# Kernel optimization log

Measured on AMD Instinct MI355X. Metric: run time of the kernel, lower is better.

## Reference

```python
import jax, jax.numpy as jnp
import numpy as np

DIM = 3072
HEADS = 24
HEAD_DIM = 128
SEQ = 4096
BATCH = 1
EPS = 1e-6


def setup_inputs() -> dict:
    key = jax.random.key(0)
    ks = jax.random.split(key, 12)
    s = 1.0 / np.sqrt(DIM)
    return {
        "hidden_states": jax.random.normal(ks[0], (BATCH, SEQ, DIM), dtype=jnp.float32),
        "cos": jax.random.uniform(ks[1], (SEQ, HEAD_DIM), dtype=jnp.float32, minval=-1.0, maxval=1.0),
        "sin": jax.random.uniform(ks[2], (SEQ, HEAD_DIM), dtype=jnp.float32, minval=-1.0, maxval=1.0),
        "Wq": jax.random.normal(ks[3], (DIM, HEADS * HEAD_DIM), dtype=jnp.float32) * s,
        "bq": jax.random.normal(ks[4], (HEADS * HEAD_DIM,), dtype=jnp.float32) * 0.02,
        "Wk": jax.random.normal(ks[5], (DIM, HEADS * HEAD_DIM), dtype=jnp.float32) * s,
        "bk": jax.random.normal(ks[6], (HEADS * HEAD_DIM,), dtype=jnp.float32) * 0.02,
        "Wv": jax.random.normal(ks[7], (DIM, HEADS * HEAD_DIM), dtype=jnp.float32) * s,
        "bv": jax.random.normal(ks[8], (HEADS * HEAD_DIM,), dtype=jnp.float32) * 0.02,
        "gq": jnp.ones((HEAD_DIM,), dtype=jnp.float32),
        "gk": jnp.ones((HEAD_DIM,), dtype=jnp.float32),
    }


def _rms_norm(x, g):
    # RMSNorm over last dim (head_dim), learnable scale g
    var = jnp.mean(jnp.square(x), axis=-1, keepdims=True)
    return x * jax.lax.rsqrt(var + EPS) * g


def _apply_rope(x, cos, sin):
    # x: [B, S, H, D]; cos/sin: [S, D]. Interleaved-pair rotation (Flux style).
    xr = x.reshape(*x.shape[:-1], HEAD_DIM // 2, 2)
    x_rot = jnp.stack((-xr[..., 1], xr[..., 0]), axis=-1).reshape(x.shape)
    c = cos[None, :, None, :]
    s = sin[None, :, None, :]
    return x * c + x_rot * s


def reference(hidden_states, cos, sin, Wq, bq, Wk, bk, Wv, bv, gq, gk):
    B, S, _ = hidden_states.shape
    q = (hidden_states @ Wq + bq).reshape(B, S, HEADS, HEAD_DIM)
    k = (hidden_states @ Wk + bk).reshape(B, S, HEADS, HEAD_DIM)
    v = (hidden_states @ Wv + bv).reshape(B, S, HEADS, HEAD_DIM)
    q = _apply_rope(_rms_norm(q, gq), cos, sin)
    k = _apply_rope(_rms_norm(k, gk), cos, sin)
    scale = 1.0 / jnp.sqrt(jnp.asarray(HEAD_DIM, dtype=q.dtype))
    scores = jnp.einsum("bqhd,bkhd->bhqk", q, k) * scale  # [B, H, S, S]
    probs = jax.nn.softmax(scores, axis=-1)
    out = jnp.einsum("bhqk,bkhd->bqhd", probs, v)  # [B, S, H, D]
    return out.reshape(B, S, HEADS * HEAD_DIM)
```

## Files before the change

### kernel.cpp

```cpp
#include <hip/hip_runtime.h>
#include <hip/hip_bf16.h>
#include <stdint.h>

#define DIM 3072
#define SEQ 4096
#define NH 24
#define HD 128

typedef __hip_bfloat16 bf16;
typedef __bf16 bfv8 __attribute__((ext_vector_type(8)));
typedef float f32x4 __attribute__((ext_vector_type(4)));
typedef float f32x16 __attribute__((ext_vector_type(16)));
typedef unsigned short us4 __attribute__((ext_vector_type(4)));
typedef unsigned short us8 __attribute__((ext_vector_type(8)));

template <int N> struct ic { static constexpr int value = N; };

__device__ __forceinline__ void async16(void* lds, const void* g) {
  __builtin_amdgcn_global_load_lds((const __attribute__((address_space(1))) void*)g,
                                   (__attribute__((address_space(3))) void*)lds, 16, 0, 0);
}

__device__ __forceinline__ unsigned short f2bf(float f) {
  unsigned int u = __builtin_bit_cast(unsigned int, f);
  u += 0x7fffu + ((u >> 16) & 1u);
  return (unsigned short)(u >> 16);
}
__device__ __forceinline__ float bf2f(unsigned short b) {
  return __builtin_bit_cast(float, (unsigned int)b << 16);
}
__device__ __forceinline__ unsigned int cvtpk(float lo, float hi) {
  unsigned int r;
  asm("v_cvt_pk_bf16_f32 %0, %1, %2" : "=v"(r) : "v"(lo), "v"(hi));
  return r;
}
__device__ __forceinline__ void pl32swap(unsigned int& a, unsigned int& b) {
  asm volatile("v_permlane32_swap_b32 %0, %1" : "+v"(a), "+v"(b));
}
#if __has_builtin(__builtin_amdgcn_exp2f)
__device__ __forceinline__ float fexp2(float x) { return __builtin_amdgcn_exp2f(x); }
#else
__device__ __forceinline__ float fexp2(float x) { return exp2f(x); }
#endif

#define MFMA16(a, b, c) __builtin_amdgcn_mfma_f32_16x16x32_bf16((a), (b), (c), 0, 0, 0)
#define MFMA32(a, b, c) __builtin_amdgcn_mfma_f32_32x32x16_bf16((a), (b), (c), 0, 0, 0)

__global__ __launch_bounds__(256) void k_cast(const float4* __restrict__ in,
                                              us4* __restrict__ o, int n4) {
  int i = blockIdx.x * 256 + threadIdx.x;
  if (i >= n4) return;
  float4 v = in[i];
  us4 r;
  r.x = f2bf(v.x); r.y = f2bf(v.y); r.z = f2bf(v.z); r.w = f2bf(v.w);
  o[i] = r;
}

__global__ __launch_bounds__(256) void k_transW(const float* __restrict__ W0,
    const float* __restrict__ W1, const float* __restrict__ W2,
    unsigned short* __restrict__ T0, unsigned short* __restrict__ T1,
    unsigned short* __restrict__ T2) {
  int z = blockIdx.z;
  const float* W = (z == 0) ? W0 : (z == 1) ? W1 : W2;
  unsigned short* T = (z == 0) ? T0 : (z == 1) ? T1 : T2;
  int kb = blockIdx.y * 64;
  int nb = blockIdx.x * 64;
  __shared__ float tile[64 * 64];
  int t = threadIdx.x;
#pragma unroll
  for (int p = 0; p < 4; ++p) {
    int cid = p * 256 + t;
    int row = cid >> 4, c4 = cid & 15;
    int slot = (c4 + (row >> 3)) & 15;
    float4 v = *(const float4*)&W[(size_t)(kb + row) * DIM + nb + c4 * 4];
    *(float4*)&tile[row * 64 + slot * 4] = v;
  }
  __syncthreads();
#pragma unroll
  for (int p = 0; p < 2; ++p) {
    int cid = p * 256 + t;
    int nl = cid >> 3, c8 = cid & 7;
    us8 o;
#pragma unroll
    for (int j = 0; j < 8; ++j) {
      int k = c8 * 8 + j;
      int slot = ((nl >> 2) + (k >> 3)) & 15;
      o[j] = f2bf(tile[k * 64 + slot * 4 + (nl & 3)]);
    }
    *(us8*)&T[(size_t)(nb + nl) * DIM + kb + c8 * 8] = o;
  }
}

__global__ __launch_bounds__(256, 2) void k_gemm(const unsigned short* __restrict__ A,
    const unsigned short* __restrict__ B0, const unsigned short* __restrict__ B1,
    const unsigned short* __restrict__ B2, const float* __restrict__ c0,
    const float* __restrict__ c1, const float* __restrict__ c2,
    unsigned short* __restrict__ o0, unsigned short* __restrict__ o1,
    unsigned short* __restrict__ o2) {
  const int z = blockIdx.z;
  const unsigned short* Bt = (z == 0) ? B0 : (z == 1) ? B1 : B2;
  const float* bias = (z == 0) ? c0 : (z == 1) ? c1 : c2;
  unsigned short* outp = (z == 0) ? o0 : (z == 1) ? o1 : o2;
  const int nb = blockIdx.x * 128;
  const int mb = blockIdx.y * 128;
  const int t = threadIdx.x;
  const int w = t >> 6, l = t & 63;
  const int wr = w >> 1, wc = w & 1;
  const int lq = l & 15, lg = l >> 4;
  __shared__ unsigned short lA[128 * 64];
  __shared__ unsigned short lB[128 * 64];
  f32x4 acc[4][4];
#pragma unroll
  for (int i = 0; i < 4; ++i)
#pragma unroll
    for (int j = 0; j < 4; ++j) acc[i][j] = (f32x4){0.f, 0.f, 0.f, 0.f};

  for (int kb = 0; kb < DIM; kb += 64) {
    __syncthreads();
#pragma unroll
    for (int r = 0; r < 4; ++r) {
      int row = (w * 4 + r) * 8 + (l >> 3);
      int sl = (l & 7) ^ (row & 7);
      async16(&lA[(w * 4 + r) * 512], A + (size_t)(mb + row) * DIM + kb + sl * 8);
      async16(&lB[(w * 4 + r) * 512], Bt + (size_t)(nb + row) * DIM + kb + sl * 8);
    }
    __syncthreads();
#pragma unroll
    for (int kc = 0; kc < 2; ++kc) {
      bfv8 af[4], bfv[4];
#pragma unroll
      for (int mf = 0; mf < 4; ++mf) {
        int row = wr * 64 + mf * 16 + lq;
        af[mf] = *(const bfv8*)&lA[row * 64 + (((kc * 4 + lg) ^ (row & 7)) * 8)];
      }
#pragma unroll
      for (int nf = 0; nf < 4; ++nf) {
        int row = wc * 64 + nf * 16 + lq;
        bfv[nf] = *(const bfv8*)&lB[row * 64 + (((kc * 4 + lg) ^ (row & 7)) * 8)];
      }
#pragma unroll
      for (int mf = 0; mf < 4; ++mf)
#pragma unroll
        for (int nf = 0; nf < 4; ++nf)
          acc[mf][nf] = MFMA16(af[mf], bfv[nf], acc[mf][nf]);
    }
  }
#pragma unroll
  for (int nf = 0; nf < 4; ++nf) {
    int n = nb + wc * 64 + nf * 16 + lq;
    float bv_ = bias[n];
    int hh = n >> 7, dd = n & 127;
    unsigned short* obase = outp + (size_t)hh * SEQ * HD + dd;
#pragma unroll
    for (int mf = 0; mf < 4; ++mf) {
      int srow = mb + wr * 64 + mf * 16 + lg * 4;
#pragma unroll
      for (int r = 0; r < 4; ++r)
        obase[(size_t)(srow + r) * HD] = f2bf(acc[mf][nf][r] + bv_);
    }
  }
}

__global__ __launch_bounds__(256) void k_rmsrope(unsigned short* __restrict__ qb,
    unsigned short* __restrict__ kbuf, const float* __restrict__ cosT,
    const float* __restrict__ sinT, const float* __restrict__ gq,
    const float* __restrict__ gk) {
  int rowid = blockIdx.x * 4 + (threadIdx.x >> 6);
  int l = threadIdx.x & 63;
  int which = (rowid >= NH * SEQ) ? 1 : 0;
  int r2 = which ? rowid - NH * SEQ : rowid;
  int hh = r2 >> 12;
  int s = r2 & 4095;
  unsigned short* base = (which ? kbuf : qb) + ((size_t)hh * SEQ + s) * HD + 2 * l;
  const float* g = which ? gk : gq;
  unsigned int u = *(const unsigned int*)base;
  float x0 = bf2f((unsigned short)(u & 0xffffu));
  float x1 = bf2f((unsigned short)(u >> 16));
  float ss = x0 * x0 + x1 * x1;
#pragma unroll
  for (int o = 1; o < 64; o <<= 1) ss += __shfl_xor(ss, o);
  float rr = rsqrtf(ss * (1.0f / 128.0f) + 1e-6f);
  int d0 = 2 * l;
  float c0v = cosT[s * HD + d0], c1v = cosT[s * HD + d0 + 1];
  float s0v = sinT[s * HD + d0], s1v = sinT[s * HD + d0 + 1];
  float y0 = x0 * rr * g[d0];
  float y1 = x1 * rr * g[d0 + 1];
  float o0 = y0 * c0v - y1 * s0v;
  float o1 = y1 * c1v + y0 * s1v;
  if (!which) { o0 *= 0.1275174373f; o1 *= 0.1275174373f; }
  *(unsigned int*)base = (unsigned int)f2bf(o0) | ((unsigned int)f2bf(o1) << 16);
}

__global__ __launch_bounds__(256) void k_transV(const unsigned short* __restrict__ vb,
                                                unsigned short* __restrict__ vt) {
  int hh = blockIdx.y;
  int sb = blockIdx.x * 64;
  __shared__ unsigned short tile[64 * 128];
  int t = threadIdx.x;
#pragma unroll
  for (int p = 0; p < 4; ++p) {
    int cid = p * 256 + t;
    int row = cid >> 4, c = cid & 15;
    int slot = (c + (row >> 3)) & 15;
    us8 v = *(const us8*)&vb[((size_t)hh * SEQ + sb + row) * HD + c * 8];
    *(us8*)&tile[row * 128 + slot * 8] = v;
  }
  __syncthreads();
#pragma unroll
  for (int p = 0; p < 4; ++p) {
    int cid = p * 256 + t;
    int d = cid >> 3, c8 = cid & 7;
    us8 o;
#pragma unroll
    for (int j = 0; j < 8; ++j) {
      int s = c8 * 8 + j;
      int slot = ((d >> 3) + (s >> 3)) & 15;
      o[j] = tile[s * 128 + slot * 8 + (d & 7)];
    }
    *(us8*)&vt[((size_t)hh * HD + d) * SEQ + sb + c8 * 8] = o;
  }
}

__global__ __launch_bounds__(256, 3) void k_attn(const unsigned short* __restrict__ qg,
    const unsigned short* __restrict__ kg, const unsigned short* __restrict__ vtg,
    float* __restrict__ outp) {
  const int h = blockIdx.y;
  const int qb0 = blockIdx.x * 128;
  const int t = threadIdx.x;
  const int w = t >> 6, l = t & 63;
  const int l31 = l & 31, hi = l >> 5;

  __shared__ unsigned short lKf[3 * 4096];
  __shared__ unsigned short lVf[3 * 4096];

  bfv8 qf[8];
  {
    const unsigned short* qrow = qg + ((size_t)h * SEQ + qb0 + w * 32 + l31) * HD + hi * 8;
#pragma unroll
    for (int ks = 0; ks < 8; ++ks) qf[ks] = *(const bfv8*)(qrow + ks * 16);
  }

  int kidx[8], vidx[4][2];
#pragma unroll
  for (int ks = 0; ks < 8; ++ks)
    kidx[ks] = l31 * 128 + (((ks * 2 + hi) ^ (l31 & 7) ^ ((l31 >> 3) & 1)) * 8);
#pragma unroll
  for (int dt = 0; dt < 4; ++dt)
#pragma unroll
    for (int ksub = 0; ksub < 2; ++ksub)
      vidx[dt][ksub] =
          (dt * 32 + l31) * 32 + (((ksub * 2 + hi) ^ (l31 & 3) ^ ((l31 >> 2) & 3)) * 8);

  const unsigned short *kp0, *kp1, *vp0, *vp1;
  {
    int kr0 = w * 4 + (l >> 4), kr1 = 16 + kr0;
    kp0 = kg + ((size_t)h * SEQ + kr0) * HD + (((l & 15) ^ (kr0 & 7) ^ ((kr0 >> 3) & 1)) * 8);
    kp1 = kg + ((size_t)h * SEQ + kr1) * HD + (((l & 15) ^ (kr1 & 7) ^ ((kr1 >> 3) & 1)) * 8);
    int vr0 = w * 16 + (l >> 2), vr1 = 64 + vr0;
    vp0 = vtg + ((size_t)h * HD + vr0) * SEQ + (((l & 3) ^ (vr0 & 3) ^ ((vr0 >> 2) & 3)) * 8);
    vp1 = vtg + ((size_t)h * HD + vr1) * SEQ + (((l & 3) ^ (vr1 & 3) ^ ((vr1 >> 2) & 3)) * 8);
  }

#define STAGE(B)                                                        \
  do {                                                                  \
    async16(&lKf[(B) * 4096 + w * 512], kp0);        kp0 += 32 * HD;    \
    async16(&lKf[(B) * 4096 + 2048 + w * 512], kp1); kp1 += 32 * HD;    \
    async16(&lVf[(B) * 4096 + w * 512], vp0);        vp0 += 32;         \
    async16(&lVf[(B) * 4096 + 2048 + w * 512], vp1); vp1 += 32;         \
  } while (0)

  f32x16 oacc[4];
#pragma unroll
  for (int dt = 0; dt < 4; ++dt)
#pragma unroll
    for (int r = 0; r < 16; ++r) oacc[dt][r] = 0.f;
  float l_run = 0.f;

  STAGE(0);
  STAGE(1);

  auto tile = [&](auto bufc, auto waitc, auto stagec) {
    constexpr int CUR = decltype(bufc)::value;
    constexpr int WAITN = decltype(waitc)::value;
    constexpr int DOSTAGE = decltype(stagec)::value;
    if constexpr (WAITN == 4)
      asm volatile("s_waitcnt vmcnt(4)" ::: "memory");
    else
      asm volatile("s_waitcnt vmcnt(0)" ::: "memory");
    __builtin_amdgcn_s_barrier();
    __builtin_amdgcn_sched_barrier(0);
    if constexpr (DOSTAGE) STAGE((CUR + 2) % 3);
    __builtin_amdgcn_sched_barrier(0);

    f32x16 st;
#pragma unroll
    for (int r = 0; r < 16; ++r) st[r] = 0.f;
    __builtin_amdgcn_s_setprio(1);
#pragma unroll
    for (int ks = 0; ks < 8; ++ks) {
      bfv8 kf = *(const bfv8*)&lKf[CUR * 4096 + kidx[ks]];
      st = MFMA32(kf, qf[ks], st);
    }
    __builtin_amdgcn_s_setprio(0);

#pragma unroll
    for (int r = 0; r < 16; ++r) st[r] = fexp2(st[r]);
    float s01 = st[0] + st[1], s23 = st[2] + st[3];
    float s45 = st[4] + st[5], s67 = st[6] + st[7];
    float s89 = st[8] + st[9], sab = st[10] + st[11];
    float scd = st[12] + st[13], sef = st[14] + st[15];
    float lsum = ((s01 + s23) + (s45 + s67)) + ((s89 + sab) + (scd + sef));
    lsum += __shfl_xor(lsum, 32);
    l_run += lsum;

    bfv8 pa[2];
    {
      unsigned int a0 = cvtpk(st[0], st[1]), a1 = cvtpk(st[2], st[3]);
      unsigned int b0 = cvtpk(st[4], st[5]), b1 = cvtpk(st[6], st[7]);
      unsigned int c0 = cvtpk(st[8], st[9]), c1 = cvtpk(st[10], st[11]);
      unsigned int d0 = cvtpk(st[12], st[13]), d1 = cvtpk(st[14], st[15]);
      pl32swap(a0, b0); pl32swap(a1, b1); pl32swap(c0, d0); pl32swap(c1, d1);
      pa[0] = __builtin_bit_cast(bfv8, make_uint4(a0, a1, b0, b1));
      pa[1] = __builtin_bit_cast(bfv8, make_uint4(c0, c1, d0, d1));
    }

    __builtin_amdgcn_s_setprio(1);
#pragma unroll
    for (int dt = 0; dt < 4; ++dt)
#pragma unroll
      for (int ksub = 0; ksub < 2; ++ksub) {
        bfv8 vf = *(const bfv8*)&lVf[CUR * 4096 + vidx[dt][ksub]];
        oacc[dt] = MFMA32(pa[ksub], vf, oacc[dt]);
      }
    __builtin_amdgcn_s_setprio(0);
  };

  for (int it = 0; it < 42; ++it) {
    tile(ic<0>{}, ic<4>{}, ic<1>{});
    tile(ic<1>{}, ic<4>{}, ic<1>{});
    tile(ic<2>{}, ic<4>{}, ic<1>{});
  }
  tile(ic<0>{}, ic<4>{}, ic<0>{});
  tile(ic<1>{}, ic<0>{}, ic<0>{});

  float linv = 1.0f / l_run;
#pragma unroll
  for (int r = 0; r < 16; ++r) {
    int qr = (r & 3) + 8 * (r >> 2) + 4 * hi;
    float lr = __shfl(linv, qr);
    float* orow = outp + (size_t)(qb0 + w * 32 + qr) * DIM + h * HD;
#pragma unroll
    for (int dt = 0; dt < 4; ++dt) orow[dt * 32 + l31] = oacc[dt][r] * lr;
  }
#undef STAGE
}

extern "C" void kernel_launch(void* const* d_in, const int* in_sizes, int n_in,
                              void* d_out, int out_size, void* d_ws, size_t ws_size,
                              hipStream_t stream) {
  const float* hs = (const float*)d_in[0];
  const float* cosT = (const float*)d_in[1];
  const float* sinT = (const float*)d_in[2];
  const float* Wq = (const float*)d_in[3];
  const float* bq = (const float*)d_in[4];
  const float* Wk = (const float*)d_in[5];
  const float* bk = (const float*)d_in[6];
  const float* Wv = (const float*)d_in[7];
  const float* bv = (const float*)d_in[8];
  const float* gq = (const float*)d_in[9];
  const float* gk = (const float*)d_in[10];
  float* out = (float*)d_out;

  char* ws = (char*)d_ws;
  const size_t SZ_HS = (size_t)SEQ * DIM * 2;
  const size_t SZ_W = (size_t)DIM * DIM * 2;
  const size_t SZ_HEAD = (size_t)NH * SEQ * HD * 2;
  unsigned short* hsb = (unsigned short*)ws;               ws += SZ_HS;
  unsigned short* WqT = (unsigned short*)ws;               ws += SZ_W;
  unsigned short* WkT = (unsigned short*)ws;               ws += SZ_W;
  unsigned short* WvT = (unsigned short*)ws;               ws += SZ_W;
  unsigned short* q_b = (unsigned short*)ws;               ws += SZ_HEAD;
  unsigned short* k_b = (unsigned short*)ws;               ws += SZ_HEAD;
  unsigned short* v_b = (unsigned short*)ws;               ws += SZ_HEAD;
  unsigned short* vtr = (unsigned short*)ws;               ws += SZ_HEAD;

  int n4 = SEQ * DIM / 4;
  k_cast<<<dim3(n4 / 256), dim3(256), 0, stream>>>((const float4*)hs, (us4*)hsb, n4);
  k_transW<<<dim3(48, 48, 3), dim3(256), 0, stream>>>(Wq, Wk, Wv, WqT, WkT, WvT);
  k_gemm<<<dim3(24, 32, 3), dim3(256), 0, stream>>>(hsb, WqT, WkT, WvT, bq, bk, bv,
                                                    q_b, k_b, v_b);
  k_rmsrope<<<dim3(2 * NH * SEQ / 4), dim3(256), 0, stream>>>(q_b, k_b, cosT, sinT, gq, gk);
  k_transV<<<dim3(64, 24), dim3(256), 0, stream>>>(v_b, vtr);
  k_attn<<<dim3(32, 24), dim3(256), 0, stream>>>(q_b, k_b, vtr, out);
}
```

Before: 572.7 us.

## Retile QKV GEMM to 256x256 with triple-buffered async LDS pipeline

The QKV projection GEMM moves from 128x128 tiles with 256 threads and a sync-load-sync loop to 256x256 tiles with 512 threads. It uses a K-step of 32, a three-stage async global-to-LDS ring with vmcnt waits, and a new XOR swizzle. This targets the exposed load latency and barrier stalls, and raises per-block data reuse. Separately, the attention QK^T MFMA chain is split into two independent accumulators to shorten the dependency chain. The larger tile means 576 blocks and more accumulators per thread, which risks register pressure and lower occupancy.

```diff
diff --git a/kernel.cpp b/kernel.cpp
--- a/kernel.cpp
+++ b/kernel.cpp
@@ -91,7 +91,7 @@
   }
 }
 
-__global__ __launch_bounds__(256, 2) void k_gemm(const unsigned short* __restrict__ A,
+__global__ __launch_bounds__(512, 2) void k_gemm(const unsigned short* __restrict__ A,
     const unsigned short* __restrict__ B0, const unsigned short* __restrict__ B1,
     const unsigned short* __restrict__ B2, const float* __restrict__ c0,
     const float* __restrict__ c1, const float* __restrict__ c2,
@@ -101,64 +101,107 @@
   const unsigned short* Bt = (z == 0) ? B0 : (z == 1) ? B1 : B2;
   const float* bias = (z == 0) ? c0 : (z == 1) ? c1 : c2;
   unsigned short* outp = (z == 0) ? o0 : (z == 1) ? o1 : o2;
-  const int nb = blockIdx.x * 128;
-  const int mb = blockIdx.y * 128;
-  const int t = threadIdx.x;
-  const int w = t >> 6, l = t & 63;
-  const int wr = w >> 1, wc = w & 1;
+  const int nb = blockIdx.x * 256;
+  const int mb = blockIdx.y * 256;
+  const int tid = threadIdx.x;
+  const int w = tid >> 6, l = tid & 63;
+  const int wm = w >> 2, wn = w & 3;
   const int lq = l & 15, lg = l >> 4;
-  __shared__ unsigned short lA[128 * 64];
-  __shared__ unsigned short lB[128 * 64];
-  f32x4 acc[4][4];
-#pragma unroll
-  for (int i = 0; i < 4; ++i)
+
+  __shared__ unsigned short lA[3 * 8192];
+  __shared__ unsigned short lB[3 * 8192];
+
+  const int srow0 = tid >> 2, srow1 = 128 + (tid >> 2);
+  const int sc = tid & 3;
+  const unsigned short* ap0 = A + (size_t)(mb + srow0) * DIM + ((sc ^ ((srow0 >> 1) & 3)) * 8);
+  const unsigned short* ap1 = A + (size_t)(mb + srow1) * DIM + ((sc ^ ((srow1 >> 1) & 3)) * 8);
+  const unsigned short* bp0 = Bt + (size_t)(nb + srow0) * DIM + ((sc ^ ((srow0 >> 1) & 3)) * 8);
+  const unsigned short* bp1 = Bt + (size_t)(nb + srow1) * DIM + ((sc ^ ((srow1 >> 1) & 3)) * 8);
+  const int dA0 = w * 512, dA1 = 4096 + w * 512;
+
+#define GSTAGE(B)                                              \
+  do {                                                         \
+    async16(&lA[(B) * 8192 + dA0], ap0); ap0 += 32;            \
+    async16(&lA[(B) * 8192 + dA1], ap1); ap1 += 32;            \
+    async16(&lB[(B) * 8192 + dA0], bp0); bp0 += 32;            \
+    async16(&lB[(B) * 8192 + dA1], bp1); bp1 += 32;            \
+  } while (0)
+
+  int aOff[8], bOff[4];
+#pragma unroll
+  for (int mf = 0; mf < 8; ++mf) {
+    int row = wm * 128 + mf * 16 + lq;
+    aOff[mf] = row * 32 + ((lg ^ ((row >> 1) & 3)) * 8);
+  }
+#pragma unroll
+  for (int nf = 0; nf < 4; ++nf) {
+    int row = wn * 64 + nf * 16 + lq;
+    bOff[nf] = row * 32 + ((lg ^ ((row >> 1) & 3)) * 8);
+  }
+
+  f32x4 acc[8][4];
+#pragma unroll
+  for (int i = 0; i < 8; ++i)
 #pragma unroll
     for (int j = 0; j < 4; ++j) acc[i][j] = (f32x4){0.f, 0.f, 0.f, 0.f};
 
-  for (int kb = 0; kb < DIM; kb += 64) {
-    __syncthreads();
-#pragma unroll
-    for (int r = 0; r < 4; ++r) {
-      int row = (w * 4 + r) * 8 + (l >> 3);
-      int sl = (l & 7) ^ (row & 7);
-      async16(&lA[(w * 4 + r) * 512], A + (size_t)(mb + row) * DIM + kb + sl * 8);
-      async16(&lB[(w * 4 + r) * 512], Bt + (size_t)(nb + row) * DIM + kb + sl * 8);
-    }
-    __syncthreads();
-#pragma unroll
-    for (int kc = 0; kc < 2; ++kc) {
-      bfv8 af[4], bfv[4];
-#pragma unroll
-      for (int mf = 0; mf < 4; ++mf) {
-        int row = wr * 64 + mf * 16 + lq;
-        af[mf] = *(const bfv8*)&lA[row * 64 + (((kc * 4 + lg) ^ (row & 7)) * 8)];
+  GSTAGE(0);
+  GSTAGE(1);
+
+  auto tileG = [&](auto bufc, auto waitc, auto stagec) {
+    constexpr int CUR = decltype(bufc)::value;
+    constexpr int WAITN = decltype(waitc)::value;
+    constexpr int DOSTAGE = decltype(stagec)::value;
+    if constexpr (WAITN == 4)
+      asm volatile("s_waitcnt vmcnt(4)" ::: "memory");
+    else
+      asm volatile("s_waitcnt vmcnt(0)" ::: "memory");
+    __builtin_amdgcn_s_barrier();
+    __builtin_amdgcn_sched_barrier(0);
+    if constexpr (DOSTAGE) GSTAGE((CUR + 2) % 3);
+    __builtin_amdgcn_sched_barrier(0);
+
+    bfv8 bF[4];
+#pragma unroll
+    for (int nf = 0; nf < 4; ++nf) bF[nf] = *(const bfv8*)&lB[CUR * 8192 + bOff[nf]];
+    __builtin_amdgcn_s_setprio(1);
+#pragma unroll
+    for (int mq = 0; mq < 4; ++mq) {
+      bfv8 aF0 = *(const bfv8*)&lA[CUR * 8192 + aOff[2 * mq]];
+      bfv8 aF1 = *(const bfv8*)&lA[CUR * 8192 + aOff[2 * mq + 1]];
+#pragma unroll
+      for (int nf = 0; nf < 4; ++nf) {
+        acc[2 * mq][nf] = MFMA16(aF0, bF[nf], acc[2 * mq][nf]);
+        acc[2 * mq + 1][nf] = MFMA16(aF1, bF[nf], acc[2 * mq + 1][nf]);
       }
-#pragma unroll
-      for (int nf = 0; nf < 4; ++nf) {
-        int row = wc * 64 + nf * 16 + lq;
-        bfv[nf] = *(const bfv8*)&lB[row * 64 + (((kc * 4 + lg) ^ (row & 7)) * 8)];
-      }
-#pragma unroll
-      for (int mf = 0; mf < 4; ++mf)
-#pragma unroll
-        for (int nf = 0; nf < 4; ++nf)
-          acc[mf][nf] = MFMA16(af[mf], bfv[nf], acc[mf][nf]);
-    }
-  }
+    }
+    __builtin_amdgcn_s_setprio(0);
+  };
+
+  for (int it = 0; it < 31; ++it) {
+    tileG(ic<0>{}, ic<4>{}, ic<1>{});
+    tileG(ic<1>{}, ic<4>{}, ic<1>{});
+    tileG(ic<2>{}, ic<4>{}, ic<1>{});
+  }
+  tileG(ic<0>{}, ic<4>{}, ic<1>{});
+  tileG(ic<1>{}, ic<4>{}, ic<0>{});
+  tileG(ic<2>{}, ic<0>{}, ic<0>{});
+
 #pragma unroll
   for (int nf = 0; nf < 4; ++nf) {
-    int n = nb + wc * 64 + nf * 16 + lq;
+    int n = nb + wn * 64 + nf * 16 + lq;
     float bv_ = bias[n];
     int hh = n >> 7, dd = n & 127;
     unsigned short* obase = outp + (size_t)hh * SEQ * HD + dd;
 #pragma unroll
-    for (int mf = 0; mf < 4; ++mf) {
-      int srow = mb + wr * 64 + mf * 16 + lg * 4;
+    for (int mf = 0; mf < 8; ++mf) {
+      int srow = mb + wm * 128 + mf * 16 + lg * 4;
 #pragma unroll
       for (int r = 0; r < 4; ++r)
         obase[(size_t)(srow + r) * HD] = f2bf(acc[mf][nf][r] + bv_);
     }
   }
+#undef GSTAGE
 }
 
 __global__ __launch_bounds__(256) void k_rmsrope(unsigned short* __restrict__ qb,
@@ -292,16 +335,19 @@
     if constexpr (DOSTAGE) STAGE((CUR + 2) % 3);
     __builtin_amdgcn_sched_barrier(0);
 
-    f32x16 st;
-#pragma unroll
-    for (int r = 0; r < 16; ++r) st[r] = 0.f;
+    f32x16 sa, sb;
+#pragma unroll
+    for (int r = 0; r < 16; ++r) { sa[r] = 0.f; sb[r] = 0.f; }
     __builtin_amdgcn_s_setprio(1);
 #pragma unroll
-    for (int ks = 0; ks < 8; ++ks) {
-      bfv8 kf = *(const bfv8*)&lKf[CUR * 4096 + kidx[ks]];
-      st = MFMA32(kf, qf[ks], st);
+    for (int ks = 0; ks < 4; ++ks) {
+      bfv8 kfa = *(const bfv8*)&lKf[CUR * 4096 + kidx[ks]];
+      bfv8 kfb = *(const bfv8*)&lKf[CUR * 4096 + kidx[ks + 4]];
+      sa = MFMA32(kfa, qf[ks], sa);
+      sb = MFMA32(kfb, qf[ks + 4], sb);
     }
     __builtin_amdgcn_s_setprio(0);
+    f32x16 st = sa + sb;
 
 #pragma unroll
     for (int r = 0; r < 16; ++r) st[r] = fexp2(st[r]);
@@ -387,7 +433,7 @@
   int n4 = SEQ * DIM / 4;
   k_cast<<<dim3(n4 / 256), dim3(256), 0, stream>>>((const float4*)hs, (us4*)hsb, n4);
   k_transW<<<dim3(48, 48, 3), dim3(256), 0, stream>>>(Wq, Wk, Wv, WqT, WkT, WvT);
-  k_gemm<<<dim3(24, 32, 3), dim3(256), 0, stream>>>(hsb, WqT, WkT, WvT, bq, bk, bv,
+  k_gemm<<<dim3(12, 16, 3), dim3(512), 0, stream>>>(hsb, WqT, WkT, WvT, bq, bk, bv,
                                                     q_b, k_b, v_b);
   k_rmsrope<<<dim3(2 * NH * SEQ / 4), dim3(256), 0, stream>>>(q_b, k_b, cosT, sinT, gq, gk);
   k_transV<<<dim3(64, 24), dim3(256), 0, stream>>>(v_b, vtr);
```

New measurement: 780.9 us. 1.36x slower.
